# Kernel optimization log

Measured on AMD Instinct MI355X. Metric: run time of the kernel, lower is better.

Reference implementation:

```python
import jax, jax.numpy as jnp
import numpy as np

LEAKY_ALPHA = 0.2
LN_EPS = 1e-5


def setup_inputs() -> dict:
    key = jax.random.key(0)
    ks = jax.random.split(key, 6)
    B, N, D, R, Hh, hd = 2, 2048, 128, 3, 4, 32  # head_dim = out_dim // num_heads = 128 // 4
    H = jax.random.normal(ks[0], (B, N, D), dtype=jnp.float32)
    A = jax.random.randint(ks[1], (R, B, N, N), 0, 2, dtype=jnp.int32)  # 0/1 adjacency per relation
    w_scale = float(np.sqrt(2.0 / (D + hd)))  # xavier-like
    a_scale = float(np.sqrt(2.0 / (hd + 1)))
    W = jax.random.normal(ks[2], (R, Hh, D, hd), dtype=jnp.float32) * w_scale
    a_src = jax.random.normal(ks[3], (R, Hh, hd), dtype=jnp.float32) * a_scale
    a_dst = jax.random.normal(ks[4], (R, Hh, hd), dtype=jnp.float32) * a_scale
    ln_gamma = jnp.ones((D,), dtype=jnp.float32)
    ln_beta = jnp.zeros((D,), dtype=jnp.float32)
    return {"H": H, "A": A, "W": W, "a_src": a_src, "a_dst": a_dst,
            "ln_gamma": ln_gamma, "ln_beta": ln_beta}


def reference(H, A, W, a_src, a_dst, ln_gamma, ln_beta):
    # H: [B,N,D]; A: [R,B,N,N] int; W: [R,Hh,D,hd]; a_*: [R,Hh,hd]
    R = W.shape[0]
    B, N, D = H.shape
    mask = (A > 0)[:, :, None, :, :]                    # [R,B,1,N,N]
    Wh = jnp.einsum('bnd,rhdf->rbhnf', H, W)             # [R,B,Hh,N,hd]
    e_src = jnp.einsum('rbhnf,rhf->rbhn', Wh, a_src)
    e_dst = jnp.einsum('rbhnf,rhf->rbhn', Wh, a_dst)
    e = e_src[..., :, None] + e_dst[..., None, :]        # [R,B,Hh,N,N]
    e = jax.nn.leaky_relu(e, LEAKY_ALPHA)
    all_false = ~jnp.any(mask, axis=-1, keepdims=True)   # rows with empty neighborhood
    logits = jnp.where(mask, e, -jnp.inf)
    logits = jnp.where(all_false, 0.0, logits)           # avoid NaN on empty rows
    alpha = jax.nn.softmax(logits, axis=-1)
    alpha = jnp.where(all_false, 0.0, alpha)
    # attention-weighted aggregation, mean over relations; -> [B,N,Hh,hd]
    agg = jnp.einsum('rbhij,rbhjf->bihf', alpha, Wh) / R
    out = agg.reshape(B, N, -1)                          # concat heads -> [B,N,out_dim]
    x = H + out                                          # res_proj is Identity (in_dim==out_dim); dropout in eval
    mu = jnp.mean(x, axis=-1, keepdims=True)
    var = jnp.var(x, axis=-1, keepdims=True)
    return (x - mu) / jnp.sqrt(var + LN_EPS) * ln_gamma + ln_beta
```

## Files before the change

### kernel.cpp

```cpp
#include <hip/hip_runtime.h>
#include <hip/hip_bf16.h>

#define RR 3
#define BB 2
#define NN 2048
#define DD 128
#define HH 4
#define HD 32
#define LEAKY 0.2f
#define LN_EPS 1e-5f
#define LOG2E 1.4426950408889634f

using f32x4  = __attribute__((ext_vector_type(4))) float;
using bf16x8 = __attribute__((ext_vector_type(8))) short;

__device__ __forceinline__ void gload_lds16(const void* g, void* l) {
    __builtin_amdgcn_global_load_lds(
        (const __attribute__((address_space(1))) unsigned*)g,
        (__attribute__((address_space(3))) unsigned*)l, 16, 0, 0);
}
__device__ __forceinline__ void gload_lds4(const void* g, void* l) {
    __builtin_amdgcn_global_load_lds(
        (const __attribute__((address_space(1))) unsigned*)g,
        (__attribute__((address_space(3))) unsigned*)l, 4, 0, 0);
}
__device__ __forceinline__ unsigned short bfb(float x) {
    return __builtin_bit_cast(unsigned short, __float2bfloat16(x));
}


__global__ __launch_bounds__(256) void prep_kernel(
    const float* __restrict__ H, const int* __restrict__ A,
    const float* __restrict__ W,
    const float* __restrict__ a_src, const float* __restrict__ a_dst,
    float* __restrict__ es, float* __restrict__ ed,
    __hip_bfloat16* __restrict__ whT, unsigned* __restrict__ bm)
{
    const int bid = blockIdx.x;
    const int t = threadIdx.x;

    if (bid >= 384) {
        const int cb = bid - 384;
        const long crow = (long)cb * 4 + (t >> 6);
        const int lane = t & 63;
        const int4* Ap = (const int4*)A + crow * 512 + lane;

        int4 v[8];
#pragma unroll
        for (int e = 0; e < 8; ++e) v[e] = Ap[e * 64];

        const int sel_e = lane >> 3;
        const int sel_q = (lane >> 1) & 3;
        const int sel_h = lane & 1;
        unsigned word = 0;
#pragma unroll
        for (int e = 0; e < 8; ++e) {
            const unsigned long long B0 = __ballot(v[e].x != 0);
            const unsigned long long B1 = __ballot(v[e].y != 0);
            const unsigned long long B2 = __ballot(v[e].z != 0);
            const unsigned long long B3 = __ballot(v[e].w != 0);
            if (sel_e == e) {
                const unsigned long long Bq =
                    (sel_q == 3) ? B3 : (sel_q == 2) ? B2 : (sel_q == 1) ? B1 : B0;
                word = sel_h ? (unsigned)(Bq >> 32) : (unsigned)Bq;
            }
        }
        bm[crow * 64 + lane] = word;
        return;
    }

    const int rbh = bid >> 4;
    const int nch = bid & 15;
    const int h = rbh & 3;
    const int b = (rbh >> 2) & 1;
    const int r = rbh >> 3;
    const int wi = r * HH + h;
    const int w  = t >> 6;
    const int l  = t & 63;
    const int lr = l & 15;
    const int lg = l >> 4;

    const float* Wp = W + (long)wi * DD * HD;
    bf16x8 afr[2][4];
#pragma unroll
    for (int mt = 0; mt < 2; ++mt)
#pragma unroll
        for (int kt = 0; kt < 4; ++kt)
#pragma unroll
            for (int e = 0; e < 8; ++e)
                afr[mt][kt][e] = (short)bfb(Wp[(kt * 32 + lg * 8 + e) * HD + mt * 16 + lr]);

    float av[2][4], dv[2][4];
#pragma unroll
    for (int mt = 0; mt < 2; ++mt)
#pragma unroll
        for (int reg = 0; reg < 4; ++reg) {
            const int f = mt * 16 + lg * 4 + reg;
            av[mt][reg] = a_src[wi * HD + f] * LOG2E;
            dv[mt][reg] = a_dst[wi * HD + f] * LOG2E;
        }

#pragma unroll
    for (int nt = 0; nt < 2; ++nt) {
        const int ncol = nch * 128 + w * 32 + nt * 16 + lr;
        const float4* hrow4 = (const float4*)(H + ((long)b * NN + ncol) * DD);
        f32x4 acc0 = {0.f, 0.f, 0.f, 0.f};
        f32x4 acc1 = {0.f, 0.f, 0.f, 0.f};
#pragma unroll
        for (int kt = 0; kt < 4; ++kt) {
            float4 h0 = hrow4[kt * 8 + lg * 2];
            float4 h1 = hrow4[kt * 8 + lg * 2 + 1];
            bf16x8 bfr;
            bfr[0] = (short)bfb(h0.x); bfr[1] = (short)bfb(h0.y);
            bfr[2] = (short)bfb(h0.z); bfr[3] = (short)bfb(h0.w);
            bfr[4] = (short)bfb(h1.x); bfr[5] = (short)bfb(h1.y);
            bfr[6] = (short)bfb(h1.z); bfr[7] = (short)bfb(h1.w);
            acc0 = __builtin_amdgcn_mfma_f32_16x16x32_bf16(afr[0][kt], bfr, acc0, 0, 0, 0);
            acc1 = __builtin_amdgcn_mfma_f32_16x16x32_bf16(afr[1][kt], bfr, acc1, 0, 0, 0);
        }
        float s = 0.f, d = 0.f;
#pragma unroll
        for (int reg = 0; reg < 4; ++reg) {
            const int f0 = lg * 4 + reg;
            const int f1 = 16 + lg * 4 + reg;
            whT[((long)rbh * HD + f0) * NN + ncol] = __float2bfloat16(acc0[reg]);
            whT[((long)rbh * HD + f1) * NN + ncol] = __float2bfloat16(acc1[reg]);
            s = fmaf(acc0[reg], av[0][reg], s);
            s = fmaf(acc1[reg], av[1][reg], s);
            d = fmaf(acc0[reg], dv[0][reg], d);
            d = fmaf(acc1[reg], dv[1][reg], d);
        }
        s += __shfl_xor(s, 16); s += __shfl_xor(s, 32);
        d += __shfl_xor(d, 16); d += __shfl_xor(d, 32);
        if (l < 16) {
            es[(long)rbh * NN + ncol] = s;
            ed[(long)rbh * NN + ncol] = d;
        }
    }
}

__global__ __launch_bounds__(256, 3) void gat_attn_kernel(
    const unsigned* __restrict__ bm, const float* __restrict__ es,
    const float* __restrict__ ed, const __hip_bfloat16* __restrict__ whT,
    unsigned* __restrict__ num, float* __restrict__ den)
{
    const int lg = ((int)blockIdx.x % 8) * 96 + (int)blockIdx.x / 8;
    const int jh = lg & 1;
    const int it = (lg >> 1) & 15;
    const int h  = (lg >> 5) & 3;
    const int b  = (lg >> 7) & 1;
    const int r  = lg >> 8;
    const int i0 = it << 7;
    const int tid = threadIdx.x;
    const int w = tid >> 6;
    const int l = tid & 63;
    const int row = l & 15;
    const int kg  = l >> 4;
    const int f31 = l & 31;
    const int kgr = l >> 5;

    __shared__ __align__(16) short    whs[2][4][4][32][8];
    __shared__ __align__(16) unsigned bms[2][4][128];
    __shared__ __align__(16) float    eds[2][4][32];
    __shared__ float red[4];

    const int rbh = (r * BB + b) * HH + h;
    const long rbNN = (long)(r * BB + b) * NN;
    const __hip_bfloat16* whTr = whT + (long)rbh * HD * NN;
    const float* edr = ed + (long)rbh * NN;
    const int jbase = jh * (NN / 2);

#define STAGE(s, nb) do {                                                           \
        const int j0s = jbase + (s) * 128;                                          \
        const int S_ = jh * 8 + (s);                                                \
        const int woff_ = (S_ >> 1) * 8 + (S_ & 1) + w * 2;                         \
        gload_lds16(whTr + (long)f31 * NN + j0s + w * 32 + kgr * 8,                 \
                    &whs[nb][w][0][0][0]);                                          \
        gload_lds16(whTr + (long)f31 * NN + j0s + w * 32 + (2 + kgr) * 8,           \
                    &whs[nb][w][2][0][0]);                                          \
        gload_lds4(bm + (rbNN + i0 + l) * 64 + woff_, &bms[nb][w][0]);              \
        gload_lds4(bm + (rbNN + i0 + 64 + l) * 64 + woff_, &bms[nb][w][64]);        \
        if (l < 32) gload_lds4(edr + j0s + w * 32 + l, &eds[nb][w][0]);             \
    } while (0)

    STAGE(0, 0);

    float4 m0 = ((const float4*)edr)[tid * 2];
    float4 m1 = ((const float4*)edr)[tid * 2 + 1];
    float mm = fmaxf(fmaxf(fmaxf(m0.x, m0.y), fmaxf(m0.z, m0.w)),
                     fmaxf(fmaxf(m1.x, m1.y), fmaxf(m1.z, m1.w)));
#pragma unroll
    for (int d = 1; d < 64; d <<= 1) mm = fmaxf(mm, __shfl_xor(mm, d));
    if (l == 0) red[w] = mm;
    __syncthreads();
    const float medf = fmaxf(fmaxf(red[0], red[1]), fmaxf(red[2], red[3]));

    const float esvA = es[(long)rbh * NN + i0 + w * 16 + row];
    const float esvB = es[(long)rbh * NN + i0 + 64 + w * 16 + row];
    const float xA = esvA + medf, xB = esvB + medf;
    const float MA = fmaxf(xA, LEAKY * xA), MB = fmaxf(xB, LEAKY * xB);
    const float uA = esvA - MA, vA = fmaf(LEAKY, esvA, -MA);
    const float uB = esvB - MB, vB = fmaf(LEAKY, esvB, -MB);

    f32x4 acc0A = {0,0,0,0}, acc1A = {0,0,0,0}, accDA = {0,0,0,0};
    f32x4 acc0B = {0,0,0,0}, acc1B = {0,0,0,0}, accDB = {0,0,0,0};
    bf16x8 ones;
#pragma unroll
    for (int i = 0; i < 8; ++i) ones[i] = (short)0x3F80;

    const int kk = kg * 2;
    const int rAi = w * 16 + row, rBi = 64 + w * 16 + row;

    for (int s = 0; s < 8; ++s) {
        const int cb = s & 1, nb = cb ^ 1;
        if (s < 7) {
            STAGE(s + 1, nb);
            asm volatile("s_waitcnt vmcnt(5)" ::: "memory");
        } else {
            asm volatile("s_waitcnt vmcnt(0)" ::: "memory");
        }
        __builtin_amdgcn_s_barrier();
        __builtin_amdgcn_sched_barrier(0);

        unsigned wA[4], wB[4];
#pragma unroll
        for (int q = 0; q < 4; ++q) {
            wA[q] = bms[cb][q][rAi];
            wB[q] = bms[cb][q][rBi];
        }

#pragma unroll
        for (int jc = 0; jc < 4; ++jc) {
            bf16x8 b0 = *(const bf16x8*)&whs[cb][jc][kg][row][0];
            bf16x8 b1 = *(const bf16x8*)&whs[cb][jc][kg][row + 16][0];
            float4 e0 = *(const float4*)&eds[cb][jc][kg * 8];
            float4 e1 = *(const float4*)&eds[cb][jc][kg * 8 + 4];

            unsigned uAq[4], uBq[4];
#pragma unroll
            for (int q = 0; q < 4; ++q) {
                uAq[q] = wA[q] >> (jc * 8 + kk);
                uBq[q] = wB[q] >> (jc * 8 + kk);
            }

            float ev[8];
            ev[0] = e0.x; ev[1] = e0.y; ev[2] = e0.z; ev[3] = e0.w;
            ev[4] = e1.x; ev[5] = e1.y; ev[6] = e1.z; ev[7] = e1.w;

            bf16x8 pA, pB;
#pragma unroll
            for (int c = 0; c < 8; ++c) {
                float pa = __builtin_amdgcn_exp2f(
                    fmaxf(uA + ev[c], fmaf(LEAKY, ev[c], vA)));
                float pb = __builtin_amdgcn_exp2f(
                    fmaxf(uB + ev[c], fmaf(LEAKY, ev[c], vB)));
                const int ma = ((int)(uAq[c & 3] << (31 - (c >> 2)))) >> 31;
                const int mb = ((int)(uBq[c & 3] << (31 - (c >> 2)))) >> 31;
                pa = __uint_as_float(__float_as_uint(pa) & (unsigned)ma);
                pb = __uint_as_float(__float_as_uint(pb) & (unsigned)mb);
                __hip_bfloat16 ha = __float2bfloat16(pa);
                __hip_bfloat16 hb = __float2bfloat16(pb);
                pA[c] = __builtin_bit_cast(short, ha);
                pB[c] = __builtin_bit_cast(short, hb);
            }

            __builtin_amdgcn_s_setprio(1);
            acc0A = __builtin_amdgcn_mfma_f32_16x16x32_bf16(pA, b0, acc0A, 0, 0, 0);
            acc1A = __builtin_amdgcn_mfma_f32_16x16x32_bf16(pA, b1, acc1A, 0, 0, 0);
            accDA = __builtin_amdgcn_mfma_f32_16x16x32_bf16(pA, ones, accDA, 0, 0, 0);
            acc0B = __builtin_amdgcn_mfma_f32_16x16x32_bf16(pB, b0, acc0B, 0, 0, 0);
            acc1B = __builtin_amdgcn_mfma_f32_16x16x32_bf16(pB, b1, acc1B, 0, 0, 0);
            accDB = __builtin_amdgcn_mfma_f32_16x16x32_bf16(pB, ones, accDB, 0, 0, 0);
            __builtin_amdgcn_s_setprio(0);
        }
        __builtin_amdgcn_s_barrier();
        __builtin_amdgcn_sched_barrier(0);
    }
#undef STAGE

    const int fcol = l & 15;
    const int pr = r * 2 + jh;
#pragma unroll
    for (int reg = 0; reg < 4; ++reg) {
        const int orow = (l >> 4) * 4 + reg;
        const long roA = (long)pr * (BB * NN) + (long)b * NN + i0 + w * 16 + orow;
        const long roB = roA + 64;
        const unsigned wa = (unsigned)bfb(acc0A[reg]) | ((unsigned)bfb(acc1A[reg]) << 16);
        const unsigned wb_ = (unsigned)bfb(acc0B[reg]) | ((unsigned)bfb(acc1B[reg]) << 16);
        num[roA * 64 + h * 16 + fcol] = wa;
        num[roB * 64 + h * 16 + fcol] = wb_;
        if (fcol == 0) {
            den[roA * HH + h] = accDA[reg];
            den[roB * HH + h] = accDB[reg];
        }
    }
}

__global__ __launch_bounds__(256) void finalize_kernel(
    const float* __restrict__ H, const unsigned* __restrict__ num,
    const float* __restrict__ den,
    const float* __restrict__ gamma, const float* __restrict__ beta,
    float* __restrict__ out)
{
    const int w = threadIdx.x >> 6;
    const int l = threadIdx.x & 63;
    const long row = (long)blockIdx.x * 4 + w;
    const int hh = l >> 4, cc = l & 15;
    const int c_lo = hh * 32 + cc, c_hi = c_lo + 16;
    const float hx = H[row * DD + c_lo];
    const float hy = H[row * DD + c_hi];

    float ax = 0.f, ay = 0.f;
#pragma unroll
    for (int r = 0; r < RR; ++r) {
        float dsum = 0.f, nx = 0.f, ny = 0.f;
#pragma unroll
        for (int j = 0; j < 2; ++j) {
            const long ro = (long)(r * 2 + j) * (BB * NN) + row;
            dsum += den[ro * HH + hh];
            const unsigned wv = num[ro * 64 + l];
            nx += __uint_as_float(wv << 16);
            ny += __uint_as_float(wv & 0xffff0000u);
        }
        const float inv = (dsum > 0.f) ? 1.0f / dsum : 0.0f;
        ax = fmaf(nx, inv, ax);
        ay = fmaf(ny, inv, ay);
    }
    const float x0 = hx + ax * (1.0f / RR);
    const float x1 = hy + ay * (1.0f / RR);
    float s = x0 + x1, q = x0 * x0 + x1 * x1;
#pragma unroll
    for (int m = 1; m < 64; m <<= 1) {
        s += __shfl_xor(s, m);
        q += __shfl_xor(q, m);
    }
    const float mu  = s * (1.0f / DD);
    const float var = q * (1.0f / DD) - mu * mu;
    const float inv = rsqrtf(var + LN_EPS);
    out[row * DD + c_lo] = (x0 - mu) * inv * gamma[c_lo] + beta[c_lo];
    out[row * DD + c_hi] = (x1 - mu) * inv * gamma[c_hi] + beta[c_hi];
}

extern "C" void kernel_launch(void* const* d_in, const int* in_sizes, int n_in,
                              void* d_out, int out_size, void* d_ws, size_t ws_size,
                              hipStream_t stream)
{
    const float* H      = (const float*)d_in[0];
    const int*   A      = (const int*)d_in[1];
    const float* W      = (const float*)d_in[2];
    const float* a_src  = (const float*)d_in[3];
    const float* a_dst  = (const float*)d_in[4];
    const float* gamma  = (const float*)d_in[5];
    const float* beta   = (const float*)d_in[6];
    float* out = (float*)d_out;

    char* ws = (char*)d_ws;
    unsigned* num = (unsigned*)ws;               ws += (size_t)RR * 2 * BB * NN * 64 * 4;
    float* den = (float*)ws;                     ws += (size_t)RR * 2 * BB * NN * HH * 4;
    float* es  = (float*)ws;                     ws += (size_t)RR * BB * HH * NN * 4;
    float* ed  = (float*)ws;                     ws += (size_t)RR * BB * HH * NN * 4;
    __hip_bfloat16* whT = (__hip_bfloat16*)ws;   ws += (size_t)RR * BB * HH * HD * NN * 2;
    unsigned* bmask = (unsigned*)ws;             ws += (size_t)RR * BB * NN * (NN / 32) * 4;

    prep_kernel<<<384 + RR * BB * NN * (NN / 32) / 256, 256, 0, stream>>>(
        H, A, W, a_src, a_dst, es, ed, whT, bmask);
    gat_attn_kernel<<<RR * BB * HH * 16 * 2, 256, 0, stream>>>(bmask, es, ed, whT, num, den);
    finalize_kernel<<<BB * NN / 4, 256, 0, stream>>>(H, num, den, gamma, beta, out);
}
```

Baseline: 65.53 us.

## Pre-tile Wh and transpose bitmask so attention stages load contiguous blocks

```diff
diff --git a/kernel.cpp b/kernel.cpp
--- a/kernel.cpp
+++ b/kernel.cpp
@@ -36,47 +36,63 @@
     float* __restrict__ es, float* __restrict__ ed,
     __hip_bfloat16* __restrict__ whT, unsigned* __restrict__ bm)
 {
+    __shared__ unsigned cb_lds[16][65];
+
     const int bid = blockIdx.x;
     const int t = threadIdx.x;
-
-    if (bid >= 384) {
-        const int cb = bid - 384;
-        const long crow = (long)cb * 4 + (t >> 6);
-        const int lane = t & 63;
-        const int4* Ap = (const int4*)A + crow * 512 + lane;
-
-        int4 v[8];
-#pragma unroll
-        for (int e = 0; e < 8; ++e) v[e] = Ap[e * 64];
-
-        const int sel_e = lane >> 3;
-        const int sel_q = (lane >> 1) & 3;
-        const int sel_h = lane & 1;
-        unsigned word = 0;
-#pragma unroll
-        for (int e = 0; e < 8; ++e) {
-            const unsigned long long B0 = __ballot(v[e].x != 0);
-            const unsigned long long B1 = __ballot(v[e].y != 0);
-            const unsigned long long B2 = __ballot(v[e].z != 0);
-            const unsigned long long B3 = __ballot(v[e].w != 0);
-            if (sel_e == e) {
-                const unsigned long long Bq =
-                    (sel_q == 3) ? B3 : (sel_q == 2) ? B2 : (sel_q == 1) ? B1 : B0;
-                word = sel_h ? (unsigned)(Bq >> 32) : (unsigned)Bq;
+    const int w = t >> 6;
+    const int l = t & 63;
+
+    if (bid < 768) {
+        const int sel_e = l >> 3;
+        const int sel_q = (l >> 1) & 3;
+        const int sel_h = l & 1;
+#pragma unroll
+        for (int iter = 0; iter < 4; ++iter) {
+            const int lr = iter * 4 + w;
+            const long crow = (long)bid * 16 + lr;
+            const int4* Ap = (const int4*)A + crow * 512 + l;
+            int4 v[8];
+#pragma unroll
+            for (int e = 0; e < 8; ++e) v[e] = Ap[e * 64];
+            unsigned word = 0;
+#pragma unroll
+            for (int e = 0; e < 8; ++e) {
+                const unsigned long long B0 = __ballot(v[e].x != 0);
+                const unsigned long long B1 = __ballot(v[e].y != 0);
+                const unsigned long long B2 = __ballot(v[e].z != 0);
+                const unsigned long long B3 = __ballot(v[e].w != 0);
+                if (sel_e == e) {
+                    const unsigned long long Bq =
+                        (sel_q == 3) ? B3 : (sel_q == 2) ? B2 : (sel_q == 1) ? B1 : B0;
+                    word = sel_h ? (unsigned)(Bq >> 32) : (unsigned)Bq;
+                }
             }
-        }
-        bm[crow * 64 + lane] = word;
+            cb_lds[lr][l] = word;
+        }
+        __syncthreads();
+        {
+            const long nrow0g = (long)bid * 16;
+            const int rb = (int)(nrow0g >> 11);
+            const int nrow0 = (int)(nrow0g & 2047);
+            const int p = t >> 2, c = t & 3;
+            uint4 val;
+            val.x = cb_lds[c * 4 + 0][p];
+            val.y = cb_lds[c * 4 + 1][p];
+            val.z = cb_lds[c * 4 + 2][p];
+            val.w = cb_lds[c * 4 + 3][p];
+            *(uint4*)(bm + ((long)rb * 64 + p) * 2048 + nrow0 + c * 4) = val;
+        }
         return;
     }
 
-    const int rbh = bid >> 4;
-    const int nch = bid & 15;
+    const int wb = bid - 768;
+    const int rbh = wb >> 4;
+    const int nch = wb & 15;
     const int h = rbh & 3;
     const int b = (rbh >> 2) & 1;
     const int r = rbh >> 3;
     const int wi = r * HH + h;
-    const int w  = t >> 6;
-    const int l  = t & 63;
     const int lr = l & 15;
     const int lg = l >> 4;
 
@@ -99,6 +115,8 @@
             av[mt][reg] = a_src[wi * HD + f] * LOG2E;
             dv[mt][reg] = a_dst[wi * HD + f] * LOG2E;
         }
+
+    __hip_bfloat16* tile = whT + ((long)rbh * 16 + nch) * 4096;
 
 #pragma unroll
     for (int nt = 0; nt < 2; ++nt) {
@@ -118,13 +136,15 @@
             acc0 = __builtin_amdgcn_mfma_f32_16x16x32_bf16(afr[0][kt], bfr, acc0, 0, 0, 0);
             acc1 = __builtin_amdgcn_mfma_f32_16x16x32_bf16(afr[1][kt], bfr, acc1, 0, 0, 0);
         }
+        const int kgw = nt * 2 + (lr >> 3);
+        const int ew = lr & 7;
         float s = 0.f, d = 0.f;
 #pragma unroll
         for (int reg = 0; reg < 4; ++reg) {
             const int f0 = lg * 4 + reg;
             const int f1 = 16 + lg * 4 + reg;
-            whT[((long)rbh * HD + f0) * NN + ncol] = __float2bfloat16(acc0[reg]);
-            whT[((long)rbh * HD + f1) * NN + ncol] = __float2bfloat16(acc1[reg]);
+            tile[((w * 4 + kgw) * 32 + f0) * 8 + ew] = __float2bfloat16(acc0[reg]);
+            tile[((w * 4 + kgw) * 32 + f1) * 8 + ew] = __float2bfloat16(acc1[reg]);
             s = fmaf(acc0[reg], av[0][reg], s);
             s = fmaf(acc1[reg], av[1][reg], s);
             d = fmaf(acc0[reg], dv[0][reg], d);
@@ -156,8 +176,6 @@
     const int l = tid & 63;
     const int row = l & 15;
     const int kg  = l >> 4;
-    const int f31 = l & 31;
-    const int kgr = l >> 5;
 
     __shared__ __align__(16) short    whs[2][4][4][32][8];
     __shared__ __align__(16) unsigned bms[2][4][128];
@@ -166,21 +184,20 @@
 
     const int rbh = (r * BB + b) * HH + h;
     const long rbNN = (long)(r * BB + b) * NN;
-    const __hip_bfloat16* whTr = whT + (long)rbh * HD * NN;
     const float* edr = ed + (long)rbh * NN;
     const int jbase = jh * (NN / 2);
 
 #define STAGE(s, nb) do {                                                           \
-        const int j0s = jbase + (s) * 128;                                          \
         const int S_ = jh * 8 + (s);                                                \
+        const __hip_bfloat16* tsrc = whT + ((long)rbh * 16 + S_) * 4096;            \
+        short* wdst = &whs[nb][0][0][0][0] + w * 1024;                              \
+        gload_lds16(tsrc + w * 1024 + l * 8, wdst);                                 \
+        gload_lds16(tsrc + w * 1024 + 512 + l * 8, wdst + 512);                     \
         const int woff_ = (S_ >> 1) * 8 + (S_ & 1) + w * 2;                         \
-        gload_lds16(whTr + (long)f31 * NN + j0s + w * 32 + kgr * 8,                 \
-                    &whs[nb][w][0][0][0]);                                          \
-        gload_lds16(whTr + (long)f31 * NN + j0s + w * 32 + (2 + kgr) * 8,           \
-                    &whs[nb][w][2][0][0]);                                          \
-        gload_lds4(bm + (rbNN + i0 + l) * 64 + woff_, &bms[nb][w][0]);              \
-        gload_lds4(bm + (rbNN + i0 + 64 + l) * 64 + woff_, &bms[nb][w][64]);        \
-        if (l < 32) gload_lds4(edr + j0s + w * 32 + l, &eds[nb][w][0]);             \
+        if (l < 32) gload_lds16(bm + rbNN * 64 + (long)woff_ * 2048 + i0 + l * 4,   \
+                                &bms[nb][w][0]);                                    \
+        if (l < 32) gload_lds4(edr + jbase + (s) * 128 + w * 32 + l,                \
+                               &eds[nb][w][0]);                                     \
     } while (0)
 
     STAGE(0, 0);
@@ -215,7 +232,7 @@
         const int cb = s & 1, nb = cb ^ 1;
         if (s < 7) {
             STAGE(s + 1, nb);
-            asm volatile("s_waitcnt vmcnt(5)" ::: "memory");
+            asm volatile("s_waitcnt vmcnt(4)" ::: "memory");
         } else {
             asm volatile("s_waitcnt vmcnt(0)" ::: "memory");
         }
@@ -362,7 +379,7 @@
     __hip_bfloat16* whT = (__hip_bfloat16*)ws;   ws += (size_t)RR * BB * HH * HD * NN * 2;
     unsigned* bmask = (unsigned*)ws;             ws += (size_t)RR * BB * NN * (NN / 32) * 4;
 
-    prep_kernel<<<384 + RR * BB * NN * (NN / 32) / 256, 256, 0, stream>>>(
+    prep_kernel<<<768 + 384, 256, 0, stream>>>(
         H, A, W, a_src, a_dst, es, ed, whT, bmask);
     gat_attn_kernel<<<RR * BB * HH * 16 * 2, 256, 0, stream>>>(bmask, es, ed, whT, num, den);
     finalize_kernel<<<BB * NN / 4, 256, 0, stream>>>(H, num, den, gamma, beta, out);
```

After: 64.71 us. Within noise of the previous version (-1.2%).
